# Optimization experiments

Measured on AMD Instinct MI355X. Metric: run time of the kernel, lower is better.

Reference implementation:

```python
import jax, jax.numpy as jnp
import numpy as np

VOCAB = 50257
EMB = 1024
H = 1024
LAYERS = 2
B = 64
S = 512


def gru_cell(x, h, w_ih, w_hh, b_ih, b_hh):
    # PyTorch GRUCell math. x:[B,in], h:[B,H], w_ih:[3H,in], w_hh:[3H,H]
    gi = x @ w_ih.T + b_ih            # [B,3H]
    gh = h @ w_hh.T + b_hh            # [B,3H]
    i_r, i_z, i_n = jnp.split(gi, 3, axis=1)
    h_r, h_z, h_n = jnp.split(gh, 3, axis=1)
    r = jax.nn.sigmoid(i_r + h_r)
    z = jax.nn.sigmoid(i_z + h_z)
    n = jnp.tanh(i_n + r * h_n)
    return (1.0 - z) * n + z * h


def setup_inputs() -> dict:
    key = jax.random.key(0)
    ks = jax.random.split(key, 16)
    s = 0.02
    inp = {
        "input_step": jax.random.randint(ks[0], (1, B), 0, VOCAB),
        "last_hidden": jax.random.normal(ks[1], (LAYERS, B, H), jnp.float32),
        "encoder_outputs": jax.random.normal(ks[2], (S, B, H), jnp.float32),
        "emb_table": jax.random.normal(ks[3], (VOCAB, EMB), jnp.float32) * s,
        "w_ih0": jax.random.normal(ks[4], (3 * H, EMB), jnp.float32) * s,
        "w_hh0": jax.random.normal(ks[5], (3 * H, H), jnp.float32) * s,
        "b_ih0": jnp.zeros((3 * H,), jnp.float32),
        "b_hh0": jnp.zeros((3 * H,), jnp.float32),
        "w_ih1": jax.random.normal(ks[6], (3 * H, H), jnp.float32) * s,
        "w_hh1": jax.random.normal(ks[7], (3 * H, H), jnp.float32) * s,
        "b_ih1": jnp.zeros((3 * H,), jnp.float32),
        "b_hh1": jnp.zeros((3 * H,), jnp.float32),
        "concat_w": jax.random.normal(ks[8], (H, 2 * H), jnp.float32) * s,
        "concat_b": jnp.zeros((H,), jnp.float32),
        "out_w": jax.random.normal(ks[9], (VOCAB, H), jnp.float32) * s,
        "out_b": jnp.zeros((VOCAB,), jnp.float32),
    }
    return inp


def reference(input_step, last_hidden, encoder_outputs, emb_table,
              w_ih0, w_hh0, b_ih0, b_hh0, w_ih1, w_hh1, b_ih1, b_hh1,
              concat_w, concat_b, out_w, out_b):
    # embedding (dropout=0 / eval mode)
    x = emb_table[input_step[0]]                       # [B,EMB]
    # 2-layer GRU, single time step
    h0 = gru_cell(x, last_hidden[0], w_ih0, w_hh0, b_ih0, b_hh0)   # [B,H]
    h1 = gru_cell(h0, last_hidden[1], w_ih1, w_hh1, b_ih1, b_hh1)  # [B,H]
    rnn_output = h1                                    # [B,H]
    hidden = jnp.stack([h0, h1], axis=0)               # [LAYERS,B,H]
    # Luong dot attention: scores [S,B] -> softmax over S per batch
    scores = jnp.einsum('bh,sbh->bs', rnn_output, encoder_outputs)  # [B,S]
    attn = jax.nn.softmax(scores, axis=1)              # [B,S]
    context = jnp.einsum('bs,sbh->bh', attn, encoder_outputs)       # [B,H]
    concat_in = jnp.concatenate([rnn_output, context], axis=1)      # [B,2H]
    concat_out = jnp.tanh(concat_in @ concat_w.T + concat_b)        # [B,H]
    logits = concat_out @ out_w.T + out_b              # [B,VOCAB]
    output = jax.nn.softmax(logits, axis=1)
    return (output, hidden)
```

## Files before the change

kernel.cpp:

```cpp
#include <hip/hip_runtime.h>
#include <hip/hip_bf16.h>
#include <math.h>

#define VOCAB 50257
#define EMB   1024
#define HID   1024
#define BATCH 64
#define SEQ   512
#define LOGITS_LD 50304
#define SCH   16
#define NCHUNK (SEQ / SCH)

typedef __attribute__((ext_vector_type(8))) short bf16x8;
typedef __attribute__((ext_vector_type(4))) float f32x4;

__device__ inline short f2bf(float x) {
    __hip_bfloat16 h = __float2bfloat16(x);
    return *reinterpret_cast<short*>(&h);
}

template <int ADD_BIAS, int KSLEN>
__global__ __launch_bounds__(256) void gemm_sk(
    const ushort* __restrict__ A0, const float* __restrict__ W0,
    const float* __restrict__ bias0, float* __restrict__ C0, int N0,
    const ushort* __restrict__ A1, const float* __restrict__ W1,
    const float* __restrict__ bias1, float* __restrict__ C1, int N1,
    int K, int ldc)
{
    const ushort* A   = blockIdx.y ? A1 : A0;
    const float*  W   = blockIdx.y ? W1 : W0;
    const float*  bia = blockIdx.y ? bias1 : bias0;
    const int     N   = blockIdx.y ? N1 : N0;
    float* C = (blockIdx.y ? C1 : C0) + (size_t)blockIdx.z * 64 * ldc;

    const int lane = threadIdx.x & 63;
    const int wv   = threadIdx.x >> 6;
    const int rowi = lane & 15;
    const int kgi  = lane >> 4;
    const int col  = blockIdx.x * 64 + wv * 16 + rowi;
    const int wcol = min(col, N - 1);

    const float*  wp = W + (size_t)wcol * K + (size_t)blockIdx.z * KSLEN + kgi * 8;
    const ushort* ap = A + (size_t)rowi * K + (size_t)blockIdx.z * KSLEN + kgi * 8;

    f32x4 acc[4] = {};

    float4 wa = *reinterpret_cast<const float4*>(wp);
    float4 wb = *reinterpret_cast<const float4*>(wp + 4);
    bf16x8 a0 = *reinterpret_cast<const bf16x8*>(ap);
    bf16x8 a1 = *reinterpret_cast<const bf16x8*>(ap + 16 * K);
    bf16x8 a2 = *reinterpret_cast<const bf16x8*>(ap + 32 * K);
    bf16x8 a3 = *reinterpret_cast<const bf16x8*>(ap + 48 * K);

#pragma unroll 4
    for (int ks = 32; ks <= KSLEN; ks += 32) {
        float4 nwa = {}, nwb = {};
        bf16x8 n0 = {}, n1 = {}, n2 = {}, n3 = {};
        if (ks < KSLEN) {
            nwa = *reinterpret_cast<const float4*>(wp + ks);
            nwb = *reinterpret_cast<const float4*>(wp + ks + 4);
            n0 = *reinterpret_cast<const bf16x8*>(ap + ks);
            n1 = *reinterpret_cast<const bf16x8*>(ap + 16 * K + ks);
            n2 = *reinterpret_cast<const bf16x8*>(ap + 32 * K + ks);
            n3 = *reinterpret_cast<const bf16x8*>(ap + 48 * K + ks);
        }
        bf16x8 b;
        b[0] = f2bf(wa.x); b[1] = f2bf(wa.y); b[2] = f2bf(wa.z); b[3] = f2bf(wa.w);
        b[4] = f2bf(wb.x); b[5] = f2bf(wb.y); b[6] = f2bf(wb.z); b[7] = f2bf(wb.w);
        acc[0] = __builtin_amdgcn_mfma_f32_16x16x32_bf16(a0, b, acc[0], 0, 0, 0);
        acc[1] = __builtin_amdgcn_mfma_f32_16x16x32_bf16(a1, b, acc[1], 0, 0, 0);
        acc[2] = __builtin_amdgcn_mfma_f32_16x16x32_bf16(a2, b, acc[2], 0, 0, 0);
        acc[3] = __builtin_amdgcn_mfma_f32_16x16x32_bf16(a3, b, acc[3], 0, 0, 0);
        wa = nwa; wb = nwb; a0 = n0; a1 = n1; a2 = n2; a3 = n3;
    }

    if (col < N) {
        float bv = ADD_BIAS ? bia[col] : 0.0f;
#pragma unroll
        for (int mt = 0; mt < 4; ++mt)
#pragma unroll
            for (int r = 0; r < 4; ++r) {
                int row = mt * 16 + kgi * 4 + r;
                C[(size_t)row * ldc + col] = acc[mt][r] + bv;
            }
    }
}

__global__ __launch_bounds__(256) void prep_k(
    const int* __restrict__ idx, const float* __restrict__ emb,
    const float* __restrict__ lh, ushort* __restrict__ x_bf,
    ushort* __restrict__ lh_bf)
{
    int i = blockIdx.x * 256 + threadIdx.x;
    if (i < 65536) {
        int b = i >> 10, e = i & 1023;
        x_bf[i] = (ushort)f2bf(emb[(size_t)idx[b] * EMB + e]);
    } else {
        int k = i - 65536;
        lh_bf[k] = (ushort)f2bf(lh[k]);
    }
}

__global__ __launch_bounds__(256) void gru_gate4_k(
    const float* __restrict__ pgi, const float* __restrict__ pgh,
    const float* __restrict__ b_ih, const float* __restrict__ b_hh,
    const float* __restrict__ hprev, float* __restrict__ out_hidden,
    ushort* __restrict__ h_bf, ushort* __restrict__ ci_bf)
{
    int i = blockIdx.x * 256 + threadIdx.x;
    int b = i >> 10, j = i & 1023;
    size_t base = (size_t)b * 3072 + j;
    float ir = b_ih[j], iz = b_ih[j + 1024], in_ = b_ih[j + 2048];
    float hr = b_hh[j], hz = b_hh[j + 1024], hn  = b_hh[j + 2048];
#pragma unroll
    for (int z = 0; z < 4; ++z) {
        size_t o = (size_t)z * 64 * 3072 + base;
        ir += pgi[o]; iz += pgi[o + 1024]; in_ += pgi[o + 2048];
        hr += pgh[o]; hz += pgh[o + 1024]; hn  += pgh[o + 2048];
    }
    float r = 1.0f / (1.0f + expf(-(ir + hr)));
    float z = 1.0f / (1.0f + expf(-(iz + hz)));
    float n = tanhf(in_ + r * hn);
    float v = (1.0f - z) * n + z * hprev[i];
    out_hidden[i] = v;
    if (h_bf)  h_bf[i] = (ushort)f2bf(v);
    if (ci_bf) ci_bf[(size_t)b * 2048 + j] = (ushort)f2bf(v);
}

__global__ __launch_bounds__(256) void attn_fused_k(
    const float* __restrict__ h1, const float* __restrict__ enc,
    float* __restrict__ pctx, float* __restrict__ pm, float* __restrict__ ps)
{
    const int b = blockIdx.y, ck = blockIdx.x;
    __shared__ float hs[HID];
    __shared__ float es[SCH][HID];
    __shared__ float sc[SCH];
    const int tid = threadIdx.x, wv = tid >> 6, lane = tid & 63;

    ((float4*)hs)[tid] = ((const float4*)(h1 + (size_t)b * HID))[tid];
    const float* ebase = enc + ((size_t)(ck * SCH) * BATCH + b) * HID;
#pragma unroll
    for (int i = 0; i < SCH; ++i) {
        int idx = tid + i * 256;
        int r = idx >> 8, c = idx & 255;
        ((float4*)es[r])[c] = ((const float4*)(ebase + (size_t)r * BATCH * HID))[c];
    }
    __syncthreads();

#pragma unroll
    for (int i = 0; i < 4; ++i) {
        int r = wv * 4 + i;
        float acc = 0.0f;
#pragma unroll
        for (int seg = 0; seg < 4; ++seg) {
            float4 ev = ((const float4*)es[r])[lane + seg * 64];
            float4 hv = ((const float4*)hs)[lane + seg * 64];
            acc += ev.x * hv.x + ev.y * hv.y + ev.z * hv.z + ev.w * hv.w;
        }
        for (int off = 32; off; off >>= 1) acc += __shfl_down(acc, off);
        if (lane == 0) sc[r] = acc;
    }
    __syncthreads();

    float m = sc[0];
#pragma unroll
    for (int s = 1; s < SCH; ++s) m = fmaxf(m, sc[s]);
    float p[SCH];
    float sum = 0.0f;
#pragma unroll
    for (int s = 0; s < SCH; ++s) { p[s] = expf(sc[s] - m); sum += p[s]; }

    float4 cacc = {0.0f, 0.0f, 0.0f, 0.0f};
#pragma unroll
    for (int s = 0; s < SCH; ++s) {
        float4 ev = ((const float4*)es[s])[tid];
        cacc.x += p[s] * ev.x; cacc.y += p[s] * ev.y;
        cacc.z += p[s] * ev.z; cacc.w += p[s] * ev.w;
    }
    ((float4*)(pctx + ((size_t)ck * BATCH + b) * HID))[tid] = cacc;
    if (tid == 0) { pm[b * NCHUNK + ck] = m; ps[b * NCHUNK + ck] = sum; }
}

__global__ __launch_bounds__(256) void attn_comb_k(
    const float* __restrict__ pctx, const float* __restrict__ pm,
    const float* __restrict__ ps, ushort* __restrict__ ci_bf)
{
    const int b = blockIdx.x, tid = threadIdx.x;
    float m = -INFINITY;
#pragma unroll
    for (int c = 0; c < NCHUNK; ++c) m = fmaxf(m, pm[b * NCHUNK + c]);
    float w[NCHUNK]; float tot = 0.0f;
#pragma unroll
    for (int c = 0; c < NCHUNK; ++c) {
        w[c] = expf(pm[b * NCHUNK + c] - m);
        tot += ps[b * NCHUNK + c] * w[c];
    }
    float inv = 1.0f / tot;
    float4 acc = {0.0f, 0.0f, 0.0f, 0.0f};
#pragma unroll
    for (int c = 0; c < NCHUNK; ++c) {
        float4 v = ((const float4*)(pctx + ((size_t)c * BATCH + b) * HID))[tid];
        acc.x += w[c] * v.x; acc.y += w[c] * v.y;
        acc.z += w[c] * v.z; acc.w += w[c] * v.w;
    }
    ushort* o = ci_bf + (size_t)b * 2048 + 1024 + tid * 4;
    o[0] = (ushort)f2bf(acc.x * inv); o[1] = (ushort)f2bf(acc.y * inv);
    o[2] = (ushort)f2bf(acc.z * inv); o[3] = (ushort)f2bf(acc.w * inv);
}

__global__ __launch_bounds__(256) void concat_comb_k(
    const float* __restrict__ pco, const float* __restrict__ bias,
    ushort* __restrict__ co_bf)
{
    int i = blockIdx.x * 256 + threadIdx.x;
    int j = i & 1023;
    float v = bias[j];
#pragma unroll
    for (int z = 0; z < 8; ++z) v += pco[(size_t)z * 65536 + i];
    co_bf[i] = (ushort)f2bf(tanhf(v));
}

#define VCHUNK 6284
__global__ __launch_bounds__(256) void stats_part_k(
    const float* __restrict__ logits, float* __restrict__ vmax,
    float* __restrict__ vsum, int ldc)
{
    int b = blockIdx.y, ch = blockIdx.x;
    int v0 = ch * VCHUNK;
    int v1 = min(v0 + VCHUNK, VOCAB);
    const float* row = logits + (size_t)b * ldc;
    float m = -INFINITY;
    for (int v = v0 + threadIdx.x; v < v1; v += 256) m = fmaxf(m, row[v]);
    __shared__ float red[4];
    for (int off = 32; off; off >>= 1) m = fmaxf(m, __shfl_xor(m, off));
    int wave = threadIdx.x >> 6, lane = threadIdx.x & 63;
    if (lane == 0) red[wave] = m;
    __syncthreads();
    m = fmaxf(fmaxf(red[0], red[1]), fmaxf(red[2], red[3]));
    float ssum = 0.0f;
    for (int v = v0 + threadIdx.x; v < v1; v += 256) ssum += expf(row[v] - m);
    for (int off = 32; off; off >>= 1) ssum += __shfl_xor(ssum, off);
    __syncthreads();
    if (lane == 0) red[wave] = ssum;
    __syncthreads();
    if (threadIdx.x == 0) {
        vmax[b * 8 + ch] = m;
        vsum[b * 8 + ch] = red[0] + red[1] + red[2] + red[3];
    }
}

__global__ __launch_bounds__(256) void softmax_v_k(
    const float* __restrict__ logits, const float* __restrict__ vmax,
    const float* __restrict__ vsum, float* __restrict__ out, int ldc)
{
    int b = blockIdx.y;
    float m = -INFINITY;
#pragma unroll
    for (int i = 0; i < 8; ++i) m = fmaxf(m, vmax[b * 8 + i]);
    float tot = 0.0f;
#pragma unroll
    for (int i = 0; i < 8; ++i) tot += vsum[b * 8 + i] * expf(vmax[b * 8 + i] - m);
    float inv = 1.0f / tot;
    int v = blockIdx.x * 1024 + threadIdx.x * 4;
    if (v + 3 < VOCAB) {
        float4 lv = *reinterpret_cast<const float4*>(logits + (size_t)b * ldc + v);
        float4 o;
        o.x = expf(lv.x - m) * inv; o.y = expf(lv.y - m) * inv;
        o.z = expf(lv.z - m) * inv; o.w = expf(lv.w - m) * inv;
        *reinterpret_cast<float4*>(out + (size_t)b * VOCAB + v) = o;
    } else {
        for (int k = 0; k < 4 && v + k < VOCAB; ++k)
            out[(size_t)b * VOCAB + v + k] = expf(logits[(size_t)b * ldc + v + k] - m) * inv;
    }
}

extern "C" void kernel_launch(void* const* d_in, const int* in_sizes, int n_in,
                              void* d_out, int out_size, void* d_ws, size_t ws_size,
                              hipStream_t stream)
{
    const int*   input_step  = (const int*)  d_in[0];
    const float* last_hidden = (const float*)d_in[1];
    const float* enc         = (const float*)d_in[2];
    const float* emb         = (const float*)d_in[3];
    const float* w_ih0       = (const float*)d_in[4];
    const float* w_hh0       = (const float*)d_in[5];
    const float* b_ih0       = (const float*)d_in[6];
    const float* b_hh0       = (const float*)d_in[7];
    const float* w_ih1       = (const float*)d_in[8];
    const float* w_hh1       = (const float*)d_in[9];
    const float* b_ih1       = (const float*)d_in[10];
    const float* b_hh1       = (const float*)d_in[11];
    const float* concat_w    = (const float*)d_in[12];
    const float* concat_b    = (const float*)d_in[13];
    const float* out_w       = (const float*)d_in[14];
    const float* out_b       = (const float*)d_in[15];

    float* out = (float*)d_out;
    float* out_probs  = out;
    float* out_hidden = out + (size_t)BATCH * VOCAB;

    float* ws = (float*)d_ws;
    float* pgi    = ws;
    float* pgh    = pgi    + 4 * 64 * 3072;
    float* pctx   = pgh    + 4 * 64 * 3072;
    float* pco    = pctx   + NCHUNK * 64 * 1024;
    float* pm     = pco    + 8 * 64 * 1024;
    float* ps     = pm     + 64 * NCHUNK;
    float* vmax   = ps     + 64 * NCHUNK;
    float* vsum   = vmax   + 64 * 8;
    float* logits = vsum   + 64 * 8;
    ushort* x_bf  = (ushort*)(logits + (size_t)64 * LOGITS_LD);
    ushort* lh_bf = x_bf  + 64 * 1024;
    ushort* h0_bf = lh_bf + 2 * 64 * 1024;
    ushort* ci_bf = h0_bf + 64 * 1024;
    ushort* co_bf = ci_bf + 64 * 2048;

    prep_k<<<768, 256, 0, stream>>>(input_step, emb, last_hidden, x_bf, lh_bf);

    gemm_sk<0, 256><<<dim3(48, 2, 4), 256, 0, stream>>>(
        x_bf,  w_ih0, nullptr, pgi, 3 * HID,
        lh_bf, w_hh0, nullptr, pgh, 3 * HID, EMB, 3 * HID);
    gru_gate4_k<<<256, 256, 0, stream>>>(pgi, pgh, b_ih0, b_hh0, last_hidden,
                                         out_hidden, h0_bf, nullptr);

    gemm_sk<0, 256><<<dim3(48, 2, 4), 256, 0, stream>>>(
        h0_bf,             w_ih1, nullptr, pgi, 3 * HID,
        lh_bf + 64 * 1024, w_hh1, nullptr, pgh, 3 * HID, HID, 3 * HID);
    gru_gate4_k<<<256, 256, 0, stream>>>(pgi, pgh, b_ih1, b_hh1, last_hidden + 64 * HID,
                                         out_hidden + 64 * HID, nullptr, ci_bf);

    attn_fused_k<<<dim3(NCHUNK, BATCH), 256, 0, stream>>>(
        out_hidden + 64 * HID, enc, pctx, pm, ps);
    attn_comb_k<<<BATCH, 256, 0, stream>>>(pctx, pm, ps, ci_bf);

    gemm_sk<0, 256><<<dim3(16, 1, 8), 256, 0, stream>>>(
        ci_bf, concat_w, nullptr, pco, HID,
        ci_bf, concat_w, nullptr, pco, HID, 2 * HID, HID);
    concat_comb_k<<<256, 256, 0, stream>>>(pco, concat_b, co_bf);

    gemm_sk<1, 1024><<<dim3(786, 1, 1), 256, 0, stream>>>(
        co_bf, out_w, out_b, logits, VOCAB,
        co_bf, out_w, out_b, logits, VOCAB, HID, LOGITS_LD);

    stats_part_k<<<dim3(8, BATCH), 256, 0, stream>>>(logits, vmax, vsum, LOGITS_LD);
    softmax_v_k<<<dim3((VOCAB + 1023) / 1024, BATCH), 256, 0, stream>>>(
        logits, vmax, vsum, out_probs, LOGITS_LD);
}
```

Baseline: 211.6 us.

## Fuse embedding gather into GEMM, hoist layer-1 hidden GEMM, drop bf16 prep

Removes the prep kernel by having the GEMM read fp32 activations directly and convert them to bf16 in registers, with the embedding gather done through an index pointer. The layer-1 recurrent GEMM (w_hh1 on the previous hidden state) is moved into the first launch alongside the two layer-0 GEMMs, so only the w_ih1 GEMM remains on the serial path, now with deeper split-K. Blocks shrink to 128 threads covering 32 columns, and workspace buffers are aliased to save memory. The cost is that activations are read as fp32, doubling their bandwidth, plus extra per-lane conversions, and the output GEMM gets twice as many blocks.

```diff
diff --git a/kernel.cpp b/kernel.cpp
--- a/kernel.cpp
+++ b/kernel.cpp
@@ -19,93 +19,97 @@
     return *reinterpret_cast<short*>(&h);
 }
 
-template <int ADD_BIAS, int KSLEN>
-__global__ __launch_bounds__(256) void gemm_sk(
-    const ushort* __restrict__ A0, const float* __restrict__ W0,
-    const float* __restrict__ bias0, float* __restrict__ C0, int N0,
-    const ushort* __restrict__ A1, const float* __restrict__ W1,
-    const float* __restrict__ bias1, float* __restrict__ C1, int N1,
-    int K, int ldc)
-{
-    const ushort* A   = blockIdx.y ? A1 : A0;
-    const float*  W   = blockIdx.y ? W1 : W0;
-    const float*  bia = blockIdx.y ? bias1 : bias0;
-    const int     N   = blockIdx.y ? N1 : N0;
-    float* C = (blockIdx.y ? C1 : C0) + (size_t)blockIdx.z * 64 * ldc;
+__device__ inline bf16x8 cvt8(const float4& a, const float4& b) {
+    bf16x8 r;
+    r[0] = f2bf(a.x); r[1] = f2bf(a.y); r[2] = f2bf(a.z); r[3] = f2bf(a.w);
+    r[4] = f2bf(b.x); r[5] = f2bf(b.y); r[6] = f2bf(b.z); r[7] = f2bf(b.w);
+    return r;
+}
+
+struct Prob {
+    const float* A;
+    const int*   gidx;
+    const float* W;
+    const float* bias;
+    float*       C;
+    int N, K, ldc;
+};
+
+template <int KSLEN, int ADD_BIAS>
+__global__ __launch_bounds__(128) void gemm_k(Prob p0, Prob p1, Prob p2)
+{
+    Prob P = (blockIdx.y == 0) ? p0 : ((blockIdx.y == 1) ? p1 : p2);
 
     const int lane = threadIdx.x & 63;
     const int wv   = threadIdx.x >> 6;
     const int rowi = lane & 15;
     const int kgi  = lane >> 4;
-    const int col  = blockIdx.x * 64 + wv * 16 + rowi;
-    const int wcol = min(col, N - 1);
-
-    const float*  wp = W + (size_t)wcol * K + (size_t)blockIdx.z * KSLEN + kgi * 8;
-    const ushort* ap = A + (size_t)rowi * K + (size_t)blockIdx.z * KSLEN + kgi * 8;
+    const int col  = blockIdx.x * 32 + wv * 16 + rowi;
+    const int wcol = min(col, P.N - 1);
+    const int kbase = blockIdx.z * KSLEN + kgi * 8;
+
+    const float* wp = P.W + (size_t)wcol * P.K + kbase;
+    const float* ap[4];
+#pragma unroll
+    for (int mt = 0; mt < 4; ++mt) {
+        int r  = rowi + mt * 16;
+        int ar = P.gidx ? P.gidx[r] : r;
+        ap[mt] = P.A + (size_t)ar * P.K + kbase;
+    }
 
     f32x4 acc[4] = {};
 
-    float4 wa = *reinterpret_cast<const float4*>(wp);
-    float4 wb = *reinterpret_cast<const float4*>(wp + 4);
-    bf16x8 a0 = *reinterpret_cast<const bf16x8*>(ap);
-    bf16x8 a1 = *reinterpret_cast<const bf16x8*>(ap + 16 * K);
-    bf16x8 a2 = *reinterpret_cast<const bf16x8*>(ap + 32 * K);
-    bf16x8 a3 = *reinterpret_cast<const bf16x8*>(ap + 48 * K);
-
-#pragma unroll 4
+    float4 wa = *(const float4*)wp;
+    float4 wb = *(const float4*)(wp + 4);
+    float4 aa[4], ab[4];
+#pragma unroll
+    for (int mt = 0; mt < 4; ++mt) {
+        aa[mt] = *(const float4*)ap[mt];
+        ab[mt] = *(const float4*)(ap[mt] + 4);
+    }
+
+#pragma unroll
     for (int ks = 32; ks <= KSLEN; ks += 32) {
-        float4 nwa = {}, nwb = {};
-        bf16x8 n0 = {}, n1 = {}, n2 = {}, n3 = {};
+        float4 nwa = {}, nwb = {}, naa[4] = {}, nab[4] = {};
         if (ks < KSLEN) {
-            nwa = *reinterpret_cast<const float4*>(wp + ks);
-            nwb = *reinterpret_cast<const float4*>(wp + ks + 4);
-            n0 = *reinterpret_cast<const bf16x8*>(ap + ks);
-            n1 = *reinterpret_cast<const bf16x8*>(ap + 16 * K + ks);
-            n2 = *reinterpret_cast<const bf16x8*>(ap + 32 * K + ks);
-            n3 = *reinterpret_cast<const bf16x8*>(ap + 48 * K + ks);
+            nwa = *(const float4*)(wp + ks);
+            nwb = *(const float4*)(wp + ks + 4);
+#pragma unroll
+            for (int mt = 0; mt < 4; ++mt) {
+                naa[mt] = *(const float4*)(ap[mt] + ks);
+                nab[mt] = *(const float4*)(ap[mt] + ks + 4);
+            }
         }
-        bf16x8 b;
-        b[0] = f2bf(wa.x); b[1] = f2bf(wa.y); b[2] = f2bf(wa.z); b[3] = f2bf(wa.w);
-        b[4] = f2bf(wb.x); b[5] = f2bf(wb.y); b[6] = f2bf(wb.z); b[7] = f2bf(wb.w);
-        acc[0] = __builtin_amdgcn_mfma_f32_16x16x32_bf16(a0, b, acc[0], 0, 0, 0);
-        acc[1] = __builtin_amdgcn_mfma_f32_16x16x32_bf16(a1, b, acc[1], 0, 0, 0);
-        acc[2] = __builtin_amdgcn_mfma_f32_16x16x32_bf16(a2, b, acc[2], 0, 0, 0);
-        acc[3] = __builtin_amdgcn_mfma_f32_16x16x32_bf16(a3, b, acc[3], 0, 0, 0);
-        wa = nwa; wb = nwb; a0 = n0; a1 = n1; a2 = n2; a3 = n3;
-    }
-
-    if (col < N) {
-        float bv = ADD_BIAS ? bia[col] : 0.0f;
+        bf16x8 b = cvt8(wa, wb);
+#pragma unroll
+        for (int mt = 0; mt < 4; ++mt) {
+            bf16x8 a = cvt8(aa[mt], ab[mt]);
+            acc[mt] = __builtin_amdgcn_mfma_f32_16x16x32_bf16(a, b, acc[mt], 0, 0, 0);
+        }
+        wa = nwa; wb = nwb;
+#pragma unroll
+        for (int mt = 0; mt < 4; ++mt) { aa[mt] = naa[mt]; ab[mt] = nab[mt]; }
+    }
+
+    if (col < P.N) {
+        float bv = ADD_BIAS ? P.bias[col] : 0.0f;
+        float* C = P.C + (size_t)blockIdx.z * 64 * P.ldc;
 #pragma unroll
         for (int mt = 0; mt < 4; ++mt)
 #pragma unroll
             for (int r = 0; r < 4; ++r) {
                 int row = mt * 16 + kgi * 4 + r;
-                C[(size_t)row * ldc + col] = acc[mt][r] + bv;
+                C[(size_t)row * P.ldc + col] = acc[mt][r] + bv;
             }
     }
 }
 
-__global__ __launch_bounds__(256) void prep_k(
-    const int* __restrict__ idx, const float* __restrict__ emb,
-    const float* __restrict__ lh, ushort* __restrict__ x_bf,
-    ushort* __restrict__ lh_bf)
-{
-    int i = blockIdx.x * 256 + threadIdx.x;
-    if (i < 65536) {
-        int b = i >> 10, e = i & 1023;
-        x_bf[i] = (ushort)f2bf(emb[(size_t)idx[b] * EMB + e]);
-    } else {
-        int k = i - 65536;
-        lh_bf[k] = (ushort)f2bf(lh[k]);
-    }
-}
-
-__global__ __launch_bounds__(256) void gru_gate4_k(
+template <int NZI, int NZH>
+__global__ __launch_bounds__(256) void gru_gate_k(
     const float* __restrict__ pgi, const float* __restrict__ pgh,
     const float* __restrict__ b_ih, const float* __restrict__ b_hh,
     const float* __restrict__ hprev, float* __restrict__ out_hidden,
-    ushort* __restrict__ h_bf, ushort* __restrict__ ci_bf)
+    float* __restrict__ h_out, float* __restrict__ ci)
 {
     int i = blockIdx.x * 256 + threadIdx.x;
     int b = i >> 10, j = i & 1023;
@@ -113,9 +117,13 @@
     float ir = b_ih[j], iz = b_ih[j + 1024], in_ = b_ih[j + 2048];
     float hr = b_hh[j], hz = b_hh[j + 1024], hn  = b_hh[j + 2048];
 #pragma unroll
-    for (int z = 0; z < 4; ++z) {
+    for (int z = 0; z < NZI; ++z) {
         size_t o = (size_t)z * 64 * 3072 + base;
         ir += pgi[o]; iz += pgi[o + 1024]; in_ += pgi[o + 2048];
+    }
+#pragma unroll
+    for (int z = 0; z < NZH; ++z) {
+        size_t o = (size_t)z * 64 * 3072 + base;
         hr += pgh[o]; hz += pgh[o + 1024]; hn  += pgh[o + 2048];
     }
     float r = 1.0f / (1.0f + expf(-(ir + hr)));
@@ -123,8 +131,8 @@
     float n = tanhf(in_ + r * hn);
     float v = (1.0f - z) * n + z * hprev[i];
     out_hidden[i] = v;
-    if (h_bf)  h_bf[i] = (ushort)f2bf(v);
-    if (ci_bf) ci_bf[(size_t)b * 2048 + j] = (ushort)f2bf(v);
+    if (h_out) h_out[i] = v;
+    if (ci)    ci[(size_t)b * 2048 + j] = v;
 }
 
 __global__ __launch_bounds__(256) void attn_fused_k(
@@ -183,7 +191,7 @@
 
 __global__ __launch_bounds__(256) void attn_comb_k(
     const float* __restrict__ pctx, const float* __restrict__ pm,
-    const float* __restrict__ ps, ushort* __restrict__ ci_bf)
+    const float* __restrict__ ps, float* __restrict__ ci)
 {
     const int b = blockIdx.x, tid = threadIdx.x;
     float m = -INFINITY;
@@ -203,21 +211,20 @@
         acc.x += w[c] * v.x; acc.y += w[c] * v.y;
         acc.z += w[c] * v.z; acc.w += w[c] * v.w;
     }
-    ushort* o = ci_bf + (size_t)b * 2048 + 1024 + tid * 4;
-    o[0] = (ushort)f2bf(acc.x * inv); o[1] = (ushort)f2bf(acc.y * inv);
-    o[2] = (ushort)f2bf(acc.z * inv); o[3] = (ushort)f2bf(acc.w * inv);
+    float4 o = {acc.x * inv, acc.y * inv, acc.z * inv, acc.w * inv};
+    ((float4*)(ci + (size_t)b * 2048 + 1024))[tid] = o;
 }
 
 __global__ __launch_bounds__(256) void concat_comb_k(
     const float* __restrict__ pco, const float* __restrict__ bias,
-    ushort* __restrict__ co_bf)
+    float* __restrict__ co)
 {
     int i = blockIdx.x * 256 + threadIdx.x;
     int j = i & 1023;
     float v = bias[j];
 #pragma unroll
     for (int z = 0; z < 8; ++z) v += pco[(size_t)z * 65536 + i];
-    co_bf[i] = (ushort)f2bf(tanhf(v));
+    co[i] = tanhf(v);
 }
 
 #define VCHUNK 6284
@@ -299,48 +306,49 @@
     float* out_probs  = out;
     float* out_hidden = out + (size_t)BATCH * VOCAB;
 
-    float* ws = (float*)d_ws;
-    float* pgi    = ws;
-    float* pgh    = pgi    + 4 * 64 * 3072;
-    float* pctx   = pgh    + 4 * 64 * 3072;
-    float* pco    = pctx   + NCHUNK * 64 * 1024;
-    float* pm     = pco    + 8 * 64 * 1024;
-    float* ps     = pm     + 64 * NCHUNK;
-    float* vmax   = ps     + 64 * NCHUNK;
-    float* vsum   = vmax   + 64 * 8;
-    float* logits = vsum   + 64 * 8;
-    ushort* x_bf  = (ushort*)(logits + (size_t)64 * LOGITS_LD);
-    ushort* lh_bf = x_bf  + 64 * 1024;
-    ushort* h0_bf = lh_bf + 2 * 64 * 1024;
-    ushort* ci_bf = h0_bf + 64 * 1024;
-    ushort* co_bf = ci_bf + 64 * 2048;
-
-    prep_k<<<768, 256, 0, stream>>>(input_step, emb, last_hidden, x_bf, lh_bf);
-
-    gemm_sk<0, 256><<<dim3(48, 2, 4), 256, 0, stream>>>(
-        x_bf,  w_ih0, nullptr, pgi, 3 * HID,
-        lh_bf, w_hh0, nullptr, pgh, 3 * HID, EMB, 3 * HID);
-    gru_gate4_k<<<256, 256, 0, stream>>>(pgi, pgh, b_ih0, b_hh0, last_hidden,
-                                         out_hidden, h0_bf, nullptr);
-
-    gemm_sk<0, 256><<<dim3(48, 2, 4), 256, 0, stream>>>(
-        h0_bf,             w_ih1, nullptr, pgi, 3 * HID,
-        lh_bf + 64 * 1024, w_hh1, nullptr, pgh, 3 * HID, HID, 3 * HID);
-    gru_gate4_k<<<256, 256, 0, stream>>>(pgi, pgh, b_ih1, b_hh1, last_hidden + 64 * HID,
-                                         out_hidden + 64 * HID, nullptr, ci_bf);
+    float* ws   = (float*)d_ws;
+    float* big  = ws;
+    float* pgi0 = big;
+    float* pgh0 = big + 786432;
+    float* pgh1 = big + 1572864;
+    float* pgi1 = big;
+    float* pctx = big;
+    float* pco  = big;
+    float* logits = ws + 2359296;
+    float* ci   = logits + (size_t)64 * LOGITS_LD;
+    float* h0   = ci + 131072;
+    float* co   = h0 + 65536;
+    float* pm   = co + 65536;
+    float* ps   = pm + 2048;
+    float* vmax = ps + 2048;
+    float* vsum = vmax + 512;
+
+    Prob P0 = { emb,         input_step, w_ih0, nullptr, pgi0, 3 * HID, EMB, 3 * HID };
+    Prob P1 = { last_hidden, nullptr,    w_hh0, nullptr, pgh0, 3 * HID, HID, 3 * HID };
+    Prob P2 = { last_hidden + 64 * HID, nullptr, w_hh1, nullptr, pgh1, 3 * HID, HID, 3 * HID };
+
+    gemm_k<256, 0><<<dim3(96, 3, 4), 128, 0, stream>>>(P0, P1, P2);
+
+    gru_gate_k<4, 4><<<256, 256, 0, stream>>>(pgi0, pgh0, b_ih0, b_hh0, last_hidden,
+                                              out_hidden, h0, nullptr);
+
+    Prob PB = { h0, nullptr, w_ih1, nullptr, pgi1, 3 * HID, HID, 3 * HID };
+    gemm_k<128, 0><<<dim3(96, 1, 8), 128, 0, stream>>>(PB, PB, PB);
+
+    gru_gate_k<8, 4><<<256, 256, 0, stream>>>(pgi1, pgh1, b_ih1, b_hh1,
+                                              last_hidden + 64 * HID,
+                                              out_hidden + 64 * HID, nullptr, ci);
 
     attn_fused_k<<<dim3(NCHUNK, BATCH), 256, 0, stream>>>(
         out_hidden + 64 * HID, enc, pctx, pm, ps);
-    attn_comb_k<<<BATCH, 256, 0, stream>>>(pctx, pm, ps, ci_bf);
-
-    gemm_sk<0, 256><<<dim3(16, 1, 8), 256, 0, stream>>>(
-        ci_bf, concat_w, nullptr, pco, HID,
-        ci_bf, concat_w, nullptr, pco, HID, 2 * HID, HID);
-    concat_comb_k<<<256, 256, 0, stream>>>(pco, concat_b, co_bf);
-
-    gemm_sk<1, 1024><<<dim3(786, 1, 1), 256, 0, stream>>>(
-        co_bf, out_w, out_b, logits, VOCAB,
-        co_bf, out_w, out_b, logits, VOCAB, HID, LOGITS_LD);
+    attn_comb_k<<<BATCH, 256, 0, stream>>>(pctx, pm, ps, ci);
+
+    Prob PC = { ci, nullptr, concat_w, nullptr, pco, HID, 2 * HID, HID };
+    gemm_k<256, 0><<<dim3(32, 1, 8), 128, 0, stream>>>(PC, PC, PC);
+    concat_comb_k<<<256, 256, 0, stream>>>(pco, concat_b, co);
+
+    Prob PL = { co, nullptr, out_w, out_b, logits, VOCAB, HID, LOGITS_LD };
+    gemm_k<1024, 1><<<dim3((VOCAB + 31) / 32, 1, 1), 128, 0, stream>>>(PL, PL, PL);
 
     stats_part_k<<<dim3(8, BATCH), 256, 0, stream>>>(logits, vmax, vsum, LOGITS_LD);
     softmax_v_k<<<dim3((VOCAB + 1023) / 1024, BATCH), 256, 0, stream>>>(
```

New measurement: 244.8 us. 15.7% more time.
